# Kernel tuning notes

Hardware: AMD Instinct MI355X
Metric: run time of the kernel (lower is better)

## Reference

```python
import jax, jax.numpy as jnp
import numpy as np

B, N, M, K, C = 2, 4096, 4096, 32, 64
RADIUS = 0.08


def _ball_query(d2, radius, k):
    # d2: (B, N, M) squared distances. Returns (B, N, k) int32 indices of the
    # first k in-radius neighbors (in index order); empty slots are filled with
    # the first found neighbor (or 0 if none), matching standard ball_query.
    m = d2.shape[-1]
    mask = d2 < radius * radius
    ar = jnp.arange(m, dtype=jnp.int32)
    key = jnp.where(mask, ar, ar + m)          # in-radius indices sort first
    neg_vals, _ = jax.lax.top_k(-key, k)       # k smallest keys
    vals = -neg_vals
    valid = vals < m
    raw = vals % m
    fill = raw[..., :1]                        # first neighbor (0 if none)
    return jnp.where(valid, raw, fill)


def setup_inputs() -> dict:
    key = jax.random.key(0)
    ks = jax.random.split(key, 9)
    points = jax.random.uniform(ks[0], (B, 3, N), dtype=jnp.float32)
    knnpoints = jax.random.uniform(ks[1], (B, 3, M), dtype=jnp.float32)
    feat = jax.random.normal(ks[2], (B, C, M), dtype=jnp.float32)
    w1 = jax.random.normal(ks[3], (128, C + 4), dtype=jnp.float32) * 0.05
    b1 = jnp.zeros((128,), jnp.float32)
    w2 = jax.random.normal(ks[4], (64, 128), dtype=jnp.float32) * 0.05
    b2 = jnp.zeros((64,), jnp.float32)
    w3 = jax.random.normal(ks[5], (64, 64), dtype=jnp.float32) * 0.05
    b3 = jnp.zeros((64,), jnp.float32)
    return {"points": points, "knnpoints": knnpoints, "feat": feat,
            "w1": w1, "b1": b1, "w2": w2, "b2": b2, "w3": w3, "b3": b3}


def reference(points, knnpoints, feat, w1, b1, w2, b2, w3, b3):
    # pairwise squared distances (B, N, M), computed once and reused by
    # ball_query and ChamferLoss
    pe = jnp.sum(points ** 2, axis=1)                       # (B, N)
    ke = jnp.sum(knnpoints ** 2, axis=1)                    # (B, M)
    cross = jnp.einsum('bdn,bdm->bnm', points, knnpoints)
    d2 = jnp.maximum(pe[:, :, None] + ke[:, None, :] - 2.0 * cross, 0.0)

    idx = _ball_query(jax.lax.stop_gradient(d2), RADIUS, K)  # (B, N, K)

    # gather neighbor coords / features: knnpoints[j, :, idx[j]]
    nb = jax.vmap(lambda p, i: p[:, i])(knnpoints, idx)      # (B, 3, N, K)
    nf = jax.vmap(lambda f, i: f[:, i])(feat, idx)           # (B, C, N, K)

    # relation features (neighbor_feature): diff + squared distance
    diff = nb - points[:, :, :, None]                        # (B, 3, N, K)
    dist = jnp.sum(diff ** 2, axis=1, keepdims=True)         # (B, 1, N, K)
    x = jnp.concatenate([nf, diff, dist], axis=1)            # (B, C+4, N, K)

    # SharedMLP: 1x1 conv stacks + ReLU
    h = jax.nn.relu(jnp.einsum('oc,bcnk->bonk', w1, x) + b1[None, :, None, None])
    h = jax.nn.relu(jnp.einsum('oc,bcnk->bonk', w2, h) + b2[None, :, None, None])
    h = jax.nn.relu(jnp.einsum('oc,bcnk->bonk', w3, h) + b3[None, :, None, None])
    agg = jnp.sum(h, axis=3)                                 # (B, 64, N)

    # ChamferLoss between points and knnpoints
    cd = jnp.sqrt(1e-6 + d2)
    loss = jnp.min(cd, axis=1).mean() + jnp.min(cd, axis=2).mean()
    return agg, loss
```

## Files before the change

kernel.cpp:

```cpp
#include <hip/hip_runtime.h>
#include <cstdint>

#define BB 2
#define NN 4096
#define MM 4096
#define KK 32
#define CC 64
#define R2C 0.0064f

typedef _Float16 v8h __attribute__((ext_vector_type(8)));
typedef _Float16 v4h __attribute__((ext_vector_type(4)));
typedef float    v4f __attribute__((ext_vector_type(4)));

__launch_bounds__(256)
__global__ void setup_kernel(const float* __restrict__ points,
                             const float* __restrict__ knn,
                             const float* __restrict__ feat,
                             const float* __restrict__ w1,
                             const float* __restrict__ w2,
                             const float* __restrict__ w3,
                             float4* __restrict__ pointsT,
                             float4* __restrict__ knnT,
                             _Float16* __restrict__ featH,
                             _Float16* __restrict__ w1h,
                             _Float16* __restrict__ w2h,
                             _Float16* __restrict__ w3h,
                             float* __restrict__ lossbuf) {
    __shared__ float tile[64][65];
    int blk = blockIdx.x, t = threadIdx.x;
    if (blk < 64) {
        const float* src = (blk < 32) ? points : knn;
        float4* dst = (blk < 32) ? pointsT : knnT;
        int i = (blk & 31) * 256 + t;
        int b = i >> 12, p = i & 4095;
        const float* base = src + (size_t)b * 3 * 4096;
        float x = base[p], y = base[4096 + p], z = base[8192 + p];
        float e = __fadd_rn(__fadd_rn(__fmul_rn(x, x), __fmul_rn(y, y)),
                            __fmul_rn(z, z));
        dst[i] = make_float4(x, y, z, e);
    } else if (blk < 192) {
        int tb = blk - 64;
        int b = tb / (MM / 64);
        int m0 = (tb % (MM / 64)) * 64;
        int mi = t & 63, cq = t >> 6;
        const float* src = feat + (size_t)b * CC * MM;
#pragma unroll
        for (int r = 0; r < 16; ++r) {
            int c = cq * 16 + r;
            tile[mi][c] = src[(size_t)c * MM + m0 + mi];
        }
        __syncthreads();
        int ci = t & 63, mq = t >> 6;
        _Float16* dst = featH + ((size_t)b * MM + m0) * CC;
#pragma unroll
        for (int r = 0; r < 16; ++r) {
            int mm = mq * 16 + r;
            dst[(size_t)mm * CC + ci] = (_Float16)tile[mm][ci];
        }
    } else if (blk < 240) {
        int tt = (blk - 192) * 256 + t;
        if (tt < 128 * 96) {
            int r = tt / 96, k = tt - r * 96;
            w1h[tt] = (_Float16)((k < 68) ? w1[r * 68 + k] : 0.0f);
        }
        if (tt < 64 * 128) w2h[tt] = (_Float16)w2[tt];
        if (tt < 64 * 64)  w3h[tt] = (_Float16)w3[tt];
    } else {
        int i = ((blk - 240) * 256 + t) * 4;
        *(float4*)(lossbuf + i) = make_float4(0.f, 0.f, 0.f, 0.f);
    }
}

__launch_bounds__(256)
__global__ void scan_kernel(const float4* __restrict__ pointsT,
                            const float4* __restrict__ knnT,
                            int* __restrict__ idx_ws,
                            float* __restrict__ lossbuf) {
    __shared__ float4 tile[1024];
    __shared__ int sidx[16][KK];
    int t = threadIdx.x;
    int w = t >> 6, lane = t & 63;
    int blk = blockIdx.x;

    if (blk < 512) {
        int pt0 = blk * 16;
        int b = pt0 >> 12;
        float4 P[4];
#pragma unroll
        for (int p = 0; p < 4; ++p) P[p] = pointsT[pt0 + 4 * w + p];
        int cnt[4] = {0, 0, 0, 0};
        float mn[4] = {1e30f, 1e30f, 1e30f, 1e30f};
        const float4* kb = knnT + (size_t)b * MM;

        for (int ch = 0; ch < 4; ++ch) {
            const float4* src = kb + ch * 1024;
            tile[t] = src[t]; tile[t + 256] = src[t + 256];
            tile[t + 512] = src[t + 512]; tile[t + 768] = src[t + 768];
            __syncthreads();
#pragma unroll 2
            for (int i = 0; i < 16; ++i) {
                float4 k4 = tile[i * 64 + lane];
                int m = ch * 1024 + i * 64 + lane;
#pragma unroll
                for (int p = 0; p < 4; ++p) {
                    float cross = __builtin_fmaf(P[p].z, k4.z,
                                  __builtin_fmaf(P[p].y, k4.y,
                                                 __fmul_rn(P[p].x, k4.x)));
                    float d2 = __fsub_rn(__fadd_rn(P[p].w, k4.w),
                                         __fmul_rn(2.0f, cross));
                    mn[p] = fminf(mn[p], fmaxf(d2, 0.0f));
                    bool hit = d2 < R2C;
                    unsigned long long mask = __ballot(hit);
                    if (hit) {
                        int pos = cnt[p] + __builtin_amdgcn_mbcnt_hi(
                                     (unsigned)(mask >> 32),
                                     __builtin_amdgcn_mbcnt_lo((unsigned)mask, 0));
                        if (pos < KK) sidx[4 * w + p][pos] = m;
                    }
                    cnt[p] += __popcll(mask);
                }
            }
            __syncthreads();
        }

        float lsum = 0.0f;
#pragma unroll
        for (int p = 0; p < 4; ++p) {
            if (lane < KK) {
                int row = 4 * w + p;
                int fillv = (cnt[p] > 0) ? sidx[row][0] : 0;
                int v = (lane < cnt[p]) ? sidx[row][lane] : fillv;
                idx_ws[((size_t)(pt0 + row)) * KK + lane] = v;
            }
            float mv = mn[p];
            for (int off = 32; off > 0; off >>= 1)
                mv = fminf(mv, __shfl_xor(mv, off));
            lsum += sqrtf(1e-6f + mv);
        }
        if (lane == 0)
            atomicAdd(lossbuf + ((blk * 4 + w) & 1023) * 8,
                      lsum * (1.0f / (BB * NN)));
    } else {
        int blk2 = blk - 512;
        int m0 = blk2 * 16;
        int b = m0 >> 12;
        float4 Kp[4];
#pragma unroll
        for (int p = 0; p < 4; ++p) Kp[p] = knnT[m0 + 4 * w + p];
        float mn[4] = {1e30f, 1e30f, 1e30f, 1e30f};
        const float4* pb = pointsT + (size_t)b * NN;

        for (int ch = 0; ch < 4; ++ch) {
            const float4* src = pb + ch * 1024;
            tile[t] = src[t]; tile[t + 256] = src[t + 256];
            tile[t + 512] = src[t + 512]; tile[t + 768] = src[t + 768];
            __syncthreads();
#pragma unroll 2
            for (int i = 0; i < 16; ++i) {
                float4 p4 = tile[i * 64 + lane];
#pragma unroll
                for (int p = 0; p < 4; ++p) {
                    float cross = __builtin_fmaf(p4.z, Kp[p].z,
                                  __builtin_fmaf(p4.y, Kp[p].y,
                                                 __fmul_rn(p4.x, Kp[p].x)));
                    float d2 = __fsub_rn(__fadd_rn(p4.w, Kp[p].w),
                                         __fmul_rn(2.0f, cross));
                    mn[p] = fminf(mn[p], fmaxf(d2, 0.0f));
                }
            }
            __syncthreads();
        }

        float lsum = 0.0f;
#pragma unroll
        for (int p = 0; p < 4; ++p) {
            float mv = mn[p];
            for (int off = 32; off > 0; off >>= 1)
                mv = fminf(mv, __shfl_xor(mv, off));
            lsum += sqrtf(1e-6f + mv);
        }
        if (lane == 0)
            atomicAdd(lossbuf + ((blk2 * 4 + w) & 1023) * 8,
                      lsum * (1.0f / (BB * MM)));
    }
}

#define TC  64
#define XS  104
#define H1S 136
#define H2S 72

__launch_bounds__(256, 4)
__global__ void mlp_kernel(const float4* __restrict__ pointsT,
                           const float4* __restrict__ knnT,
                           const _Float16* __restrict__ featH,
                           const int* __restrict__ idx_ws,
                           const _Float16* __restrict__ w1h, const float* __restrict__ b1,
                           const _Float16* __restrict__ w2h, const float* __restrict__ b2,
                           const _Float16* __restrict__ w3h, const float* __restrict__ b3,
                           const float* __restrict__ lossbuf,
                           float* __restrict__ out) {
    __shared__ __align__(16) _Float16 SM[TC * XS + TC * H1S];
    _Float16* X  = SM;
    _Float16* H2 = SM;
    _Float16* H1 = SM + TC * XS;
    __shared__ float ws4[4];

    int t = threadIdx.x;

    if (blockIdx.x == 0) {
        float s = lossbuf[t * 8] + lossbuf[(t + 256) * 8] +
                  lossbuf[(t + 512) * 8] + lossbuf[(t + 768) * 8];
        for (int off = 32; off > 0; off >>= 1) s += __shfl_xor(s, off);
        if ((t & 63) == 0) ws4[t >> 6] = s;
        __syncthreads();
        if (t == 0)
            out[(size_t)BB * 64 * NN] = ws4[0] + ws4[1] + ws4[2] + ws4[3];
    }

    int point0 = blockIdx.x * 2;
    int b = point0 >> 12;
    int n0 = point0 & (NN - 1);

    {
        int col = t >> 2, h = t & 3;
        int pl = col >> 5, kk = col & 31;
        int n = n0 + pl;
        int id = idx_ws[(((size_t)b * NN + n) << 5) + kk];
        const v8h* src = (const v8h*)(featH + ((size_t)(b * MM + id)) * CC) + h * 2;
        v8h f0 = src[0], f1 = src[1];
        v8h* dst = (v8h*)(X + col * XS) + h * 2;
        dst[0] = f0; dst[1] = f1;
        v8h mv = {(_Float16)0.f, (_Float16)0.f, (_Float16)0.f, (_Float16)0.f,
                  (_Float16)0.f, (_Float16)0.f, (_Float16)0.f, (_Float16)0.f};
        if (h == 0) {
            float4 p4 = pointsT[b * NN + n];
            float4 nb = knnT[b * MM + id];
            float dx = nb.x - p4.x, dy = nb.y - p4.y, dz = nb.z - p4.z;
            float dd = __fadd_rn(__fadd_rn(__fmul_rn(dx, dx), __fmul_rn(dy, dy)),
                                 __fmul_rn(dz, dz));
            mv[0] = (_Float16)dx; mv[1] = (_Float16)dy;
            mv[2] = (_Float16)dz; mv[3] = (_Float16)dd;
        }
        *((v8h*)(X + col * XS + 64) + h) = mv;
    }

    int w = t >> 6, l = t & 63;
    int quad = l >> 4, lc = l & 15;

    v8h a1[2][3], a2[4], a3[2];
#pragma unroll
    for (int rt = 0; rt < 2; ++rt)
#pragma unroll
        for (int ks = 0; ks < 3; ++ks)
            a1[rt][ks] = *(const v8h*)(w1h + (32 * w + 16 * rt + lc) * 96 + 32 * ks + 8 * quad);
#pragma unroll
    for (int ks = 0; ks < 4; ++ks)
        a2[ks] = *(const v8h*)(w2h + (16 * w + lc) * 128 + 32 * ks + 8 * quad);
#pragma unroll
    for (int ks = 0; ks < 2; ++ks)
        a3[ks] = *(const v8h*)(w3h + (16 * w + lc) * 64 + 32 * ks + 8 * quad);

    v4f bias1a = *(const v4f*)(b1 + 32 * w + 4 * quad);
    v4f bias1b = *(const v4f*)(b1 + 32 * w + 16 + 4 * quad);
    v4f bias2  = *(const v4f*)(b2 + 16 * w + 4 * quad);
    v4f bias3  = *(const v4f*)(b3 + 16 * w + 4 * quad);

    __syncthreads();

#pragma unroll 1
    for (int ct = 0; ct < 4; ++ct) {
        int colb = 16 * ct + lc;
        v4f acc0 = bias1a, acc1 = bias1b;
#pragma unroll
        for (int ks = 0; ks < 3; ++ks) {
            v8h bx = *(const v8h*)(X + colb * XS + 32 * ks + 8 * quad);
            acc0 = __builtin_amdgcn_mfma_f32_16x16x32_f16(a1[0][ks], bx, acc0, 0, 0, 0);
            acc1 = __builtin_amdgcn_mfma_f32_16x16x32_f16(a1[1][ks], bx, acc1, 0, 0, 0);
        }
        v4h h0, h1v;
#pragma unroll
        for (int r = 0; r < 4; ++r) {
            h0[r]  = (_Float16)fmaxf(acc0[r], 0.0f);
            h1v[r] = (_Float16)fmaxf(acc1[r], 0.0f);
        }
        *(v4h*)(H1 + colb * H1S + 32 * w + 4 * quad)      = h0;
        *(v4h*)(H1 + colb * H1S + 32 * w + 16 + 4 * quad) = h1v;
    }
    __syncthreads();

#pragma unroll 1
    for (int ct = 0; ct < 4; ++ct) {
        int colb = 16 * ct + lc;
        v4f acc = bias2;
#pragma unroll
        for (int ks = 0; ks < 4; ++ks) {
            v8h bx = *(const v8h*)(H1 + colb * H1S + 32 * ks + 8 * quad);
            acc = __builtin_amdgcn_mfma_f32_16x16x32_f16(a2[ks], bx, acc, 0, 0, 0);
        }
        v4h h;
#pragma unroll
        for (int r = 0; r < 4; ++r) h[r] = (_Float16)fmaxf(acc[r], 0.0f);
        *(v4h*)(H2 + colb * H2S + 16 * w + 4 * quad) = h;
    }
    __syncthreads();

#pragma unroll 1
    for (int p = 0; p < 2; ++p) {
        int cA = (2 * p) * 16 + lc, cB = (2 * p + 1) * 16 + lc;
        v4f accA = bias3, accB = bias3;
#pragma unroll
        for (int ks = 0; ks < 2; ++ks) {
            v8h bA = *(const v8h*)(H2 + cA * H2S + 32 * ks + 8 * quad);
            v8h bB = *(const v8h*)(H2 + cB * H2S + 32 * ks + 8 * quad);
            accA = __builtin_amdgcn_mfma_f32_16x16x32_f16(a3[ks], bA, accA, 0, 0, 0);
            accB = __builtin_amdgcn_mfma_f32_16x16x32_f16(a3[ks], bB, accB, 0, 0, 0);
        }
        v4f s;
#pragma unroll
        for (int r = 0; r < 4; ++r)
            s[r] = fmaxf(accA[r], 0.0f) + fmaxf(accB[r], 0.0f);
#pragma unroll
        for (int off = 1; off < 16; off <<= 1) {
#pragma unroll
            for (int r = 0; r < 4; ++r) s[r] += __shfl_xor(s[r], off);
        }
        if (lc == 0) {
            int n = n0 + p;
            int rowb = 16 * w + 4 * quad;
#pragma unroll
            for (int r = 0; r < 4; ++r)
                out[((size_t)(b * 64 + rowb + r)) * NN + n] = s[r];
        }
    }
}

extern "C" void kernel_launch(void* const* d_in, const int* in_sizes, int n_in,
                              void* d_out, int out_size, void* d_ws, size_t ws_size,
                              hipStream_t stream) {
    const float* points = (const float*)d_in[0];
    const float* knn    = (const float*)d_in[1];
    const float* feat   = (const float*)d_in[2];
    const float* w1 = (const float*)d_in[3];
    const float* b1 = (const float*)d_in[4];
    const float* w2 = (const float*)d_in[5];
    const float* b2 = (const float*)d_in[6];
    const float* w3 = (const float*)d_in[7];
    const float* b3 = (const float*)d_in[8];
    float* out = (float*)d_out;

    char* ws = (char*)d_ws;
    float4*    pointsT = (float4*)ws;
    float4*    knnT    = (float4*)(ws + 131072);
    _Float16*  featH   = (_Float16*)(ws + 262144);
    int*       idx_ws  = (int*)(ws + 1310720);
    _Float16*  w1h     = (_Float16*)(ws + 2359296);
    _Float16*  w2h     = (_Float16*)(ws + 2383872);
    _Float16*  w3h     = (_Float16*)(ws + 2400256);
    float*     lossbuf = (float*)(ws + 2408448);

    setup_kernel<<<248, 256, 0, stream>>>(points, knn, feat, w1, w2, w3,
                                          pointsT, knnT, featH, w1h, w2h, w3h,
                                          lossbuf);
    scan_kernel<<<1024, 256, 0, stream>>>(pointsT, knnT, idx_ws, lossbuf);
    mlp_kernel<<<(BB * NN) / 2, 256, 0, stream>>>(pointsT, knnT, featH, idx_ws,
                                                  w1h, b1, w2h, b2, w3h, b3,
                                                  lossbuf, out);
}
```

Measured before the change: 121.4 us.

## Fuse ball-query scan and MLP into one kernel with last-block loss reduction

Merges the scan and MLP kernels so each ball-query block keeps its neighbor indices in shared memory and runs the three-layer MLP over its 16 points in 8 passes. This removes the idx_ws global round trip and one kernel launch. The final loss reduction moves to whichever block increments an atomic counter last. The trade-off is fewer, heavier blocks for the MLP phase (512 blocks doing 8 sequential passes instead of 4096 small blocks), which may hurt latency hiding. The fused kernel also has a larger shared-memory footprint and uses launch bounds of 4.

```diff
diff --git a/kernel.cpp b/kernel.cpp
--- a/kernel.cpp
+++ b/kernel.cpp
@@ -11,6 +11,11 @@
 typedef _Float16 v8h __attribute__((ext_vector_type(8)));
 typedef _Float16 v4h __attribute__((ext_vector_type(4)));
 typedef float    v4f __attribute__((ext_vector_type(4)));
+
+#define TC  64
+#define XS  104
+#define H1S 136
+#define H2S 72
 
 __launch_bounds__(256)
 __global__ void setup_kernel(const float* __restrict__ points,
@@ -25,7 +30,8 @@
                              _Float16* __restrict__ w1h,
                              _Float16* __restrict__ w2h,
                              _Float16* __restrict__ w3h,
-                             float* __restrict__ lossbuf) {
+                             float* __restrict__ lossbuf,
+                             int* __restrict__ counter) {
     __shared__ float tile[64][65];
     int blk = blockIdx.x, t = threadIdx.x;
     if (blk < 64) {
@@ -68,16 +74,29 @@
     } else {
         int i = ((blk - 240) * 256 + t) * 4;
         *(float4*)(lossbuf + i) = make_float4(0.f, 0.f, 0.f, 0.f);
+        if (blk == 240 && t == 0) counter[0] = 0;
     }
 }
 
-__launch_bounds__(256)
-__global__ void scan_kernel(const float4* __restrict__ pointsT,
-                            const float4* __restrict__ knnT,
-                            int* __restrict__ idx_ws,
-                            float* __restrict__ lossbuf) {
-    __shared__ float4 tile[1024];
+__launch_bounds__(256, 4)
+__global__ void fused_kernel(const float4* __restrict__ pointsT,
+                             const float4* __restrict__ knnT,
+                             const _Float16* __restrict__ featH,
+                             const _Float16* __restrict__ w1h, const float* __restrict__ b1,
+                             const _Float16* __restrict__ w2h, const float* __restrict__ b2,
+                             const _Float16* __restrict__ w3h, const float* __restrict__ b3,
+                             float* __restrict__ lossbuf,
+                             int* __restrict__ counter,
+                             float* __restrict__ out) {
+    __shared__ __align__(16) char SM[TC * XS * 2 + TC * H1S * 2];
     __shared__ int sidx[16][KK];
+    __shared__ float ws4v[4];
+    __shared__ int rflag;
+    float4*   tile = (float4*)SM;
+    _Float16* X    = (_Float16*)SM;
+    _Float16* H2   = (_Float16*)SM;
+    _Float16* H1   = (_Float16*)SM + TC * XS;
+
     int t = threadIdx.x;
     int w = t >> 6, lane = t & 63;
     int blk = blockIdx.x;
@@ -108,7 +127,7 @@
                                                  __fmul_rn(P[p].x, k4.x)));
                     float d2 = __fsub_rn(__fadd_rn(P[p].w, k4.w),
                                          __fmul_rn(2.0f, cross));
-                    mn[p] = fminf(mn[p], fmaxf(d2, 0.0f));
+                    mn[p] = fminf(mn[p], d2);
                     bool hit = d2 < R2C;
                     unsigned long long mask = __ballot(hit);
                     if (hit) {
@@ -126,20 +145,155 @@
         float lsum = 0.0f;
 #pragma unroll
         for (int p = 0; p < 4; ++p) {
+            int row = 4 * w + p;
             if (lane < KK) {
-                int row = 4 * w + p;
                 int fillv = (cnt[p] > 0) ? sidx[row][0] : 0;
-                int v = (lane < cnt[p]) ? sidx[row][lane] : fillv;
-                idx_ws[((size_t)(pt0 + row)) * KK + lane] = v;
+                if (lane >= cnt[p]) sidx[row][lane] = fillv;
             }
             float mv = mn[p];
             for (int off = 32; off > 0; off >>= 1)
                 mv = fminf(mv, __shfl_xor(mv, off));
-            lsum += sqrtf(1e-6f + mv);
+            lsum += sqrtf(1e-6f + fmaxf(mv, 0.0f));
         }
         if (lane == 0)
             atomicAdd(lossbuf + ((blk * 4 + w) & 1023) * 8,
                       lsum * (1.0f / (BB * NN)));
+        __syncthreads();
+        if (t == 0) {
+            __threadfence();
+            rflag = (atomicAdd(counter, 1) == 1023) ? 1 : 0;
+        }
+        __syncthreads();
+        if (rflag) {
+            float s = 0.0f;
+#pragma unroll
+            for (int q = 0; q < 4; ++q)
+                s += __hip_atomic_load(lossbuf + (t + 256 * q) * 8,
+                                       __ATOMIC_RELAXED, __HIP_MEMORY_SCOPE_AGENT);
+            for (int off = 32; off > 0; off >>= 1) s += __shfl_xor(s, off);
+            if ((t & 63) == 0) ws4v[t >> 6] = s;
+            __syncthreads();
+            if (t == 0)
+                out[(size_t)BB * 64 * NN] = ws4v[0] + ws4v[1] + ws4v[2] + ws4v[3];
+        }
+
+        int quad = lane >> 4, lc = lane & 15;
+        size_t bM = (size_t)b * MM;
+        int n0 = pt0;
+
+        v8h a1[2][3], a2[4], a3[2];
+#pragma unroll
+        for (int rt = 0; rt < 2; ++rt)
+#pragma unroll
+            for (int ks = 0; ks < 3; ++ks)
+                a1[rt][ks] = *(const v8h*)(w1h + (32 * w + 16 * rt + lc) * 96 + 32 * ks + 8 * quad);
+#pragma unroll
+        for (int ks = 0; ks < 4; ++ks)
+            a2[ks] = *(const v8h*)(w2h + (16 * w + lc) * 128 + 32 * ks + 8 * quad);
+#pragma unroll
+        for (int ks = 0; ks < 2; ++ks)
+            a3[ks] = *(const v8h*)(w3h + (16 * w + lc) * 64 + 32 * ks + 8 * quad);
+
+        v4f bias1a = *(const v4f*)(b1 + 32 * w + 4 * quad);
+        v4f bias1b = *(const v4f*)(b1 + 32 * w + 16 + 4 * quad);
+        v4f bias2  = *(const v4f*)(b2 + 16 * w + 4 * quad);
+        v4f bias3  = *(const v4f*)(b3 + 16 * w + 4 * quad);
+
+        __syncthreads();
+
+#pragma unroll 1
+        for (int ps = 0; ps < 8; ++ps) {
+            {
+                int col = t >> 2, h = t & 3;
+                int pl = col >> 5, kk = col & 31;
+                int lrow = 2 * ps + pl;
+                int id = sidx[lrow][kk];
+                const v8h* src = (const v8h*)(featH + (bM + id) * CC) + h * 2;
+                v8h f0 = src[0], f1 = src[1];
+                v8h* dst = (v8h*)(X + col * XS) + h * 2;
+                dst[0] = f0; dst[1] = f1;
+                v8h mv = {(_Float16)0.f, (_Float16)0.f, (_Float16)0.f, (_Float16)0.f,
+                          (_Float16)0.f, (_Float16)0.f, (_Float16)0.f, (_Float16)0.f};
+                if (h == 0) {
+                    float4 p4 = pointsT[n0 + lrow];
+                    float4 nb = knnT[bM + id];
+                    float dx = nb.x - p4.x, dy = nb.y - p4.y, dz = nb.z - p4.z;
+                    float dd = __fadd_rn(__fadd_rn(__fmul_rn(dx, dx), __fmul_rn(dy, dy)),
+                                         __fmul_rn(dz, dz));
+                    mv[0] = (_Float16)dx; mv[1] = (_Float16)dy;
+                    mv[2] = (_Float16)dz; mv[3] = (_Float16)dd;
+                }
+                *((v8h*)(X + col * XS + 64) + h) = mv;
+            }
+            __syncthreads();
+
+#pragma unroll 1
+            for (int ct = 0; ct < 4; ++ct) {
+                int colb = 16 * ct + lc;
+                v4f acc0 = bias1a, acc1 = bias1b;
+#pragma unroll
+                for (int ks = 0; ks < 3; ++ks) {
+                    v8h bx = *(const v8h*)(X + colb * XS + 32 * ks + 8 * quad);
+                    acc0 = __builtin_amdgcn_mfma_f32_16x16x32_f16(a1[0][ks], bx, acc0, 0, 0, 0);
+                    acc1 = __builtin_amdgcn_mfma_f32_16x16x32_f16(a1[1][ks], bx, acc1, 0, 0, 0);
+                }
+                v4h h0, h1v;
+#pragma unroll
+                for (int r = 0; r < 4; ++r) {
+                    h0[r]  = (_Float16)fmaxf(acc0[r], 0.0f);
+                    h1v[r] = (_Float16)fmaxf(acc1[r], 0.0f);
+                }
+                *(v4h*)(H1 + colb * H1S + 32 * w + 4 * quad)      = h0;
+                *(v4h*)(H1 + colb * H1S + 32 * w + 16 + 4 * quad) = h1v;
+            }
+            __syncthreads();
+
+#pragma unroll 1
+            for (int ct = 0; ct < 4; ++ct) {
+                int colb = 16 * ct + lc;
+                v4f acc = bias2;
+#pragma unroll
+                for (int ks = 0; ks < 4; ++ks) {
+                    v8h bx = *(const v8h*)(H1 + colb * H1S + 32 * ks + 8 * quad);
+                    acc = __builtin_amdgcn_mfma_f32_16x16x32_f16(a2[ks], bx, acc, 0, 0, 0);
+                }
+                v4h h;
+#pragma unroll
+                for (int r = 0; r < 4; ++r) h[r] = (_Float16)fmaxf(acc[r], 0.0f);
+                *(v4h*)(H2 + colb * H2S + 16 * w + 4 * quad) = h;
+            }
+            __syncthreads();
+
+#pragma unroll 1
+            for (int p = 0; p < 2; ++p) {
+                int cA = (2 * p) * 16 + lc, cB = (2 * p + 1) * 16 + lc;
+                v4f accA = bias3, accB = bias3;
+#pragma unroll
+                for (int ks = 0; ks < 2; ++ks) {
+                    v8h bA = *(const v8h*)(H2 + cA * H2S + 32 * ks + 8 * quad);
+                    v8h bB = *(const v8h*)(H2 + cB * H2S + 32 * ks + 8 * quad);
+                    accA = __builtin_amdgcn_mfma_f32_16x16x32_f16(a3[ks], bA, accA, 0, 0, 0);
+                    accB = __builtin_amdgcn_mfma_f32_16x16x32_f16(a3[ks], bB, accB, 0, 0, 0);
+                }
+                v4f s;
+#pragma unroll
+                for (int r = 0; r < 4; ++r)
+                    s[r] = fmaxf(accA[r], 0.0f) + fmaxf(accB[r], 0.0f);
+#pragma unroll
+                for (int off = 1; off < 16; off <<= 1) {
+#pragma unroll
+                    for (int r = 0; r < 4; ++r) s[r] += __shfl_xor(s[r], off);
+                }
+                if (lc == 0) {
+                    int nloc = (n0 & (NN - 1)) + 2 * ps + p;
+                    int rowb = 16 * w + 4 * quad;
+#pragma unroll
+                    for (int r = 0; r < 4; ++r)
+                        out[((size_t)(b * 64 + rowb + r)) * NN + nloc] = s[r];
+                }
+            }
+            __syncthreads();
+        }
     } else {
         int blk2 = blk - 512;
         int m0 = blk2 * 16;
@@ -165,7 +319,7 @@
                                                  __fmul_rn(p4.x, Kp[p].x)));
                     float d2 = __fsub_rn(__fadd_rn(p4.w, Kp[p].w),
                                          __fmul_rn(2.0f, cross));
-                    mn[p] = fminf(mn[p], fmaxf(d2, 0.0f));
+                    mn[p] = fminf(mn[p], d2);
                 }
             }
             __syncthreads();
@@ -177,160 +331,28 @@
             float mv = mn[p];
             for (int off = 32; off > 0; off >>= 1)
                 mv = fminf(mv, __shfl_xor(mv, off));
-            lsum += sqrtf(1e-6f + mv);
+            lsum += sqrtf(1e-6f + fmaxf(mv, 0.0f));
         }
         if (lane == 0)
             atomicAdd(lossbuf + ((blk2 * 4 + w) & 1023) * 8,
                       lsum * (1.0f / (BB * MM)));
-    }
-}
-
-#define TC  64
-#define XS  104
-#define H1S 136
-#define H2S 72
-
-__launch_bounds__(256, 4)
-__global__ void mlp_kernel(const float4* __restrict__ pointsT,
-                           const float4* __restrict__ knnT,
-                           const _Float16* __restrict__ featH,
-                           const int* __restrict__ idx_ws,
-                           const _Float16* __restrict__ w1h, const float* __restrict__ b1,
-                           const _Float16* __restrict__ w2h, const float* __restrict__ b2,
-                           const _Float16* __restrict__ w3h, const float* __restrict__ b3,
-                           const float* __restrict__ lossbuf,
-                           float* __restrict__ out) {
-    __shared__ __align__(16) _Float16 SM[TC * XS + TC * H1S];
-    _Float16* X  = SM;
-    _Float16* H2 = SM;
-    _Float16* H1 = SM + TC * XS;
-    __shared__ float ws4[4];
-
-    int t = threadIdx.x;
-
-    if (blockIdx.x == 0) {
-        float s = lossbuf[t * 8] + lossbuf[(t + 256) * 8] +
-                  lossbuf[(t + 512) * 8] + lossbuf[(t + 768) * 8];
-        for (int off = 32; off > 0; off >>= 1) s += __shfl_xor(s, off);
-        if ((t & 63) == 0) ws4[t >> 6] = s;
-        __syncthreads();
-        if (t == 0)
-            out[(size_t)BB * 64 * NN] = ws4[0] + ws4[1] + ws4[2] + ws4[3];
-    }
-
-    int point0 = blockIdx.x * 2;
-    int b = point0 >> 12;
-    int n0 = point0 & (NN - 1);
-
-    {
-        int col = t >> 2, h = t & 3;
-        int pl = col >> 5, kk = col & 31;
-        int n = n0 + pl;
-        int id = idx_ws[(((size_t)b * NN + n) << 5) + kk];
-        const v8h* src = (const v8h*)(featH + ((size_t)(b * MM + id)) * CC) + h * 2;
-        v8h f0 = src[0], f1 = src[1];
-        v8h* dst = (v8h*)(X + col * XS) + h * 2;
-        dst[0] = f0; dst[1] = f1;
-        v8h mv = {(_Float16)0.f, (_Float16)0.f, (_Float16)0.f, (_Float16)0.f,
-                  (_Float16)0.f, (_Float16)0.f, (_Float16)0.f, (_Float16)0.f};
-        if (h == 0) {
-            float4 p4 = pointsT[b * NN + n];
-            float4 nb = knnT[b * MM + id];
-            float dx = nb.x - p4.x, dy = nb.y - p4.y, dz = nb.z - p4.z;
-            float dd = __fadd_rn(__fadd_rn(__fmul_rn(dx, dx), __fmul_rn(dy, dy)),
-                                 __fmul_rn(dz, dz));
-            mv[0] = (_Float16)dx; mv[1] = (_Float16)dy;
-            mv[2] = (_Float16)dz; mv[3] = (_Float16)dd;
-        }
-        *((v8h*)(X + col * XS + 64) + h) = mv;
-    }
-
-    int w = t >> 6, l = t & 63;
-    int quad = l >> 4, lc = l & 15;
-
-    v8h a1[2][3], a2[4], a3[2];
-#pragma unroll
-    for (int rt = 0; rt < 2; ++rt)
-#pragma unroll
-        for (int ks = 0; ks < 3; ++ks)
-            a1[rt][ks] = *(const v8h*)(w1h + (32 * w + 16 * rt + lc) * 96 + 32 * ks + 8 * quad);
-#pragma unroll
-    for (int ks = 0; ks < 4; ++ks)
-        a2[ks] = *(const v8h*)(w2h + (16 * w + lc) * 128 + 32 * ks + 8 * quad);
-#pragma unroll
-    for (int ks = 0; ks < 2; ++ks)
-        a3[ks] = *(const v8h*)(w3h + (16 * w + lc) * 64 + 32 * ks + 8 * quad);
-
-    v4f bias1a = *(const v4f*)(b1 + 32 * w + 4 * quad);
-    v4f bias1b = *(const v4f*)(b1 + 32 * w + 16 + 4 * quad);
-    v4f bias2  = *(const v4f*)(b2 + 16 * w + 4 * quad);
-    v4f bias3  = *(const v4f*)(b3 + 16 * w + 4 * quad);
-
-    __syncthreads();
-
-#pragma unroll 1
-    for (int ct = 0; ct < 4; ++ct) {
-        int colb = 16 * ct + lc;
-        v4f acc0 = bias1a, acc1 = bias1b;
-#pragma unroll
-        for (int ks = 0; ks < 3; ++ks) {
-            v8h bx = *(const v8h*)(X + colb * XS + 32 * ks + 8 * quad);
-            acc0 = __builtin_amdgcn_mfma_f32_16x16x32_f16(a1[0][ks], bx, acc0, 0, 0, 0);
-            acc1 = __builtin_amdgcn_mfma_f32_16x16x32_f16(a1[1][ks], bx, acc1, 0, 0, 0);
-        }
-        v4h h0, h1v;
-#pragma unroll
-        for (int r = 0; r < 4; ++r) {
-            h0[r]  = (_Float16)fmaxf(acc0[r], 0.0f);
-            h1v[r] = (_Float16)fmaxf(acc1[r], 0.0f);
-        }
-        *(v4h*)(H1 + colb * H1S + 32 * w + 4 * quad)      = h0;
-        *(v4h*)(H1 + colb * H1S + 32 * w + 16 + 4 * quad) = h1v;
-    }
-    __syncthreads();
-
-#pragma unroll 1
-    for (int ct = 0; ct < 4; ++ct) {
-        int colb = 16 * ct + lc;
-        v4f acc = bias2;
-#pragma unroll
-        for (int ks = 0; ks < 4; ++ks) {
-            v8h bx = *(const v8h*)(H1 + colb * H1S + 32 * ks + 8 * quad);
-            acc = __builtin_amdgcn_mfma_f32_16x16x32_f16(a2[ks], bx, acc, 0, 0, 0);
-        }
-        v4h h;
-#pragma unroll
-        for (int r = 0; r < 4; ++r) h[r] = (_Float16)fmaxf(acc[r], 0.0f);
-        *(v4h*)(H2 + colb * H2S + 16 * w + 4 * quad) = h;
-    }
-    __syncthreads();
-
-#pragma unroll 1
-    for (int p = 0; p < 2; ++p) {
-        int cA = (2 * p) * 16 + lc, cB = (2 * p + 1) * 16 + lc;
-        v4f accA = bias3, accB = bias3;
-#pragma unroll
-        for (int ks = 0; ks < 2; ++ks) {
-            v8h bA = *(const v8h*)(H2 + cA * H2S + 32 * ks + 8 * quad);
-            v8h bB = *(const v8h*)(H2 + cB * H2S + 32 * ks + 8 * quad);
-            accA = __builtin_amdgcn_mfma_f32_16x16x32_f16(a3[ks], bA, accA, 0, 0, 0);
-            accB = __builtin_amdgcn_mfma_f32_16x16x32_f16(a3[ks], bB, accB, 0, 0, 0);
-        }
-        v4f s;
-#pragma unroll
-        for (int r = 0; r < 4; ++r)
-            s[r] = fmaxf(accA[r], 0.0f) + fmaxf(accB[r], 0.0f);
-#pragma unroll
-        for (int off = 1; off < 16; off <<= 1) {
-#pragma unroll
-            for (int r = 0; r < 4; ++r) s[r] += __shfl_xor(s[r], off);
-        }
-        if (lc == 0) {
-            int n = n0 + p;
-            int rowb = 16 * w + 4 * quad;
-#pragma unroll
-            for (int r = 0; r < 4; ++r)
-                out[((size_t)(b * 64 + rowb + r)) * NN + n] = s[r];
+        __syncthreads();
+        if (t == 0) {
+            __threadfence();
+            rflag = (atomicAdd(counter, 1) == 1023) ? 1 : 0;
+        }
+        __syncthreads();
+        if (rflag) {
+            float s = 0.0f;
+#pragma unroll
+            for (int q = 0; q < 4; ++q)
+                s += __hip_atomic_load(lossbuf + (t + 256 * q) * 8,
+                                       __ATOMIC_RELAXED, __HIP_MEMORY_SCOPE_AGENT);
+            for (int off = 32; off > 0; off >>= 1) s += __shfl_xor(s, off);
+            if ((t & 63) == 0) ws4v[t >> 6] = s;
+            __syncthreads();
+            if (t == 0)
+                out[(size_t)BB * 64 * NN] = ws4v[0] + ws4v[1] + ws4v[2] + ws4v[3];
         }
     }
 }
@@ -353,17 +375,16 @@
     float4*    pointsT = (float4*)ws;
     float4*    knnT    = (float4*)(ws + 131072);
     _Float16*  featH   = (_Float16*)(ws + 262144);
-    int*       idx_ws  = (int*)(ws + 1310720);
-    _Float16*  w1h     = (_Float16*)(ws + 2359296);
-    _Float16*  w2h     = (_Float16*)(ws + 2383872);
-    _Float16*  w3h     = (_Float16*)(ws + 2400256);
-    float*     lossbuf = (float*)(ws + 2408448);
+    _Float16*  w1h     = (_Float16*)(ws + 1310720);
+    _Float16*  w2h     = (_Float16*)(ws + 1335296);
+    _Float16*  w3h     = (_Float16*)(ws + 1351680);
+    float*     lossbuf = (float*)(ws + 1359872);
+    int*       counter = (int*)(ws + 1392640);
 
     setup_kernel<<<248, 256, 0, stream>>>(points, knn, feat, w1, w2, w3,
                                           pointsT, knnT, featH, w1h, w2h, w3h,
-                                          lossbuf);
-    scan_kernel<<<1024, 256, 0, stream>>>(pointsT, knnT, idx_ws, lossbuf);
-    mlp_kernel<<<(BB * NN) / 2, 256, 0, stream>>>(pointsT, knnT, featH, idx_ws,
-                                                  w1h, b1, w2h, b2, w3h, b3,
-                                                  lossbuf, out);
+                                          lossbuf, counter);
+    fused_kernel<<<1024, 256, 0, stream>>>(pointsT, knnT, featH,
+                                           w1h, b1, w2h, b2, w3h, b3,
+                                           lossbuf, counter, out);
 }
```

Measured after the change: 130.9 us. 7.8% more time.

## Fuse setup into scan kernel and compute point norms on the fly

Applied to the files above, without the earlier changes.

Merges the setup kernel into the scan kernel, so one launch and one inter-kernel dependency go away. The transposed float4 point copies are dropped: the scan and MLP kernels now read the SoA coordinates directly and recompute squared norms per tile. The loss partials are written to distinct slots instead of atomically added, which also removes the buffer zeroing, and the clamp to zero moves after the min reduction. In exchange each scan block does extra strided loads and norm arithmetic, and the feature and weight conversion blocks now run in the same grid as the scan blocks.

```diff
diff --git a/kernel.cpp b/kernel.cpp
--- a/kernel.cpp
+++ b/kernel.cpp
@@ -12,90 +12,58 @@
 typedef _Float16 v4h __attribute__((ext_vector_type(4)));
 typedef float    v4f __attribute__((ext_vector_type(4)));
 
+#define TC  64
+#define XS  104
+#define H1S 136
+#define H2S 72
+
 __launch_bounds__(256)
-__global__ void setup_kernel(const float* __restrict__ points,
-                             const float* __restrict__ knn,
-                             const float* __restrict__ feat,
-                             const float* __restrict__ w1,
-                             const float* __restrict__ w2,
-                             const float* __restrict__ w3,
-                             float4* __restrict__ pointsT,
-                             float4* __restrict__ knnT,
-                             _Float16* __restrict__ featH,
-                             _Float16* __restrict__ w1h,
-                             _Float16* __restrict__ w2h,
-                             _Float16* __restrict__ w3h,
-                             float* __restrict__ lossbuf) {
-    __shared__ float tile[64][65];
-    int blk = blockIdx.x, t = threadIdx.x;
-    if (blk < 64) {
-        const float* src = (blk < 32) ? points : knn;
-        float4* dst = (blk < 32) ? pointsT : knnT;
-        int i = (blk & 31) * 256 + t;
-        int b = i >> 12, p = i & 4095;
-        const float* base = src + (size_t)b * 3 * 4096;
-        float x = base[p], y = base[4096 + p], z = base[8192 + p];
-        float e = __fadd_rn(__fadd_rn(__fmul_rn(x, x), __fmul_rn(y, y)),
-                            __fmul_rn(z, z));
-        dst[i] = make_float4(x, y, z, e);
-    } else if (blk < 192) {
-        int tb = blk - 64;
-        int b = tb / (MM / 64);
-        int m0 = (tb % (MM / 64)) * 64;
-        int mi = t & 63, cq = t >> 6;
-        const float* src = feat + (size_t)b * CC * MM;
-#pragma unroll
-        for (int r = 0; r < 16; ++r) {
-            int c = cq * 16 + r;
-            tile[mi][c] = src[(size_t)c * MM + m0 + mi];
-        }
-        __syncthreads();
-        int ci = t & 63, mq = t >> 6;
-        _Float16* dst = featH + ((size_t)b * MM + m0) * CC;
-#pragma unroll
-        for (int r = 0; r < 16; ++r) {
-            int mm = mq * 16 + r;
-            dst[(size_t)mm * CC + ci] = (_Float16)tile[mm][ci];
-        }
-    } else if (blk < 240) {
-        int tt = (blk - 192) * 256 + t;
-        if (tt < 128 * 96) {
-            int r = tt / 96, k = tt - r * 96;
-            w1h[tt] = (_Float16)((k < 68) ? w1[r * 68 + k] : 0.0f);
-        }
-        if (tt < 64 * 128) w2h[tt] = (_Float16)w2[tt];
-        if (tt < 64 * 64)  w3h[tt] = (_Float16)w3[tt];
-    } else {
-        int i = ((blk - 240) * 256 + t) * 4;
-        *(float4*)(lossbuf + i) = make_float4(0.f, 0.f, 0.f, 0.f);
-    }
-}
-
-__launch_bounds__(256)
-__global__ void scan_kernel(const float4* __restrict__ pointsT,
-                            const float4* __restrict__ knnT,
-                            int* __restrict__ idx_ws,
-                            float* __restrict__ lossbuf) {
-    __shared__ float4 tile[1024];
+__global__ void scan_setup_kernel(const float* __restrict__ points,
+                                  const float* __restrict__ knn,
+                                  const float* __restrict__ feat,
+                                  const float* __restrict__ w1,
+                                  const float* __restrict__ w2,
+                                  const float* __restrict__ w3,
+                                  _Float16* __restrict__ featH,
+                                  _Float16* __restrict__ w1h,
+                                  _Float16* __restrict__ w2h,
+                                  _Float16* __restrict__ w3h,
+                                  int* __restrict__ idx_ws,
+                                  float* __restrict__ lossbuf) {
+    __shared__ __align__(16) char SM[16640];
     __shared__ int sidx[16][KK];
+    float4* tile = (float4*)SM;
     int t = threadIdx.x;
     int w = t >> 6, lane = t & 63;
     int blk = blockIdx.x;
 
     if (blk < 512) {
         int pt0 = blk * 16;
-        int b = pt0 >> 12;
+        int b = blk >> 8;
+        const float* pp = points + (size_t)b * 3 * NN;
+        const float* kp = knn + (size_t)b * 3 * MM;
         float4 P[4];
 #pragma unroll
-        for (int p = 0; p < 4; ++p) P[p] = pointsT[pt0 + 4 * w + p];
+        for (int p = 0; p < 4; ++p) {
+            int nl = (pt0 & (NN - 1)) + 4 * w + p;
+            float x = pp[nl], y = pp[NN + nl], z = pp[2 * NN + nl];
+            float e = __fadd_rn(__fadd_rn(__fmul_rn(x, x), __fmul_rn(y, y)),
+                                __fmul_rn(z, z));
+            P[p] = make_float4(x, y, z, e);
+        }
         int cnt[4] = {0, 0, 0, 0};
         float mn[4] = {1e30f, 1e30f, 1e30f, 1e30f};
-        const float4* kb = knnT + (size_t)b * MM;
 
         for (int ch = 0; ch < 4; ++ch) {
-            const float4* src = kb + ch * 1024;
-            tile[t] = src[t]; tile[t + 256] = src[t + 256];
-            tile[t + 512] = src[t + 512]; tile[t + 768] = src[t + 768];
+            const float* kx = kp + ch * 1024;
+#pragma unroll
+            for (int j = 0; j < 4; ++j) {
+                int i = t + 256 * j;
+                float x = kx[i], y = kx[MM + i], z = kx[2 * MM + i];
+                float e = __fadd_rn(__fadd_rn(__fmul_rn(x, x), __fmul_rn(y, y)),
+                                    __fmul_rn(z, z));
+                tile[i] = make_float4(x, y, z, e);
+            }
             __syncthreads();
 #pragma unroll 2
             for (int i = 0; i < 16; ++i) {
@@ -108,7 +76,7 @@
                                                  __fmul_rn(P[p].x, k4.x)));
                     float d2 = __fsub_rn(__fadd_rn(P[p].w, k4.w),
                                          __fmul_rn(2.0f, cross));
-                    mn[p] = fminf(mn[p], fmaxf(d2, 0.0f));
+                    mn[p] = fminf(mn[p], d2);
                     bool hit = d2 < R2C;
                     unsigned long long mask = __ballot(hit);
                     if (hit) {
@@ -126,8 +94,8 @@
         float lsum = 0.0f;
 #pragma unroll
         for (int p = 0; p < 4; ++p) {
+            int row = 4 * w + p;
             if (lane < KK) {
-                int row = 4 * w + p;
                 int fillv = (cnt[p] > 0) ? sidx[row][0] : 0;
                 int v = (lane < cnt[p]) ? sidx[row][lane] : fillv;
                 idx_ws[((size_t)(pt0 + row)) * KK + lane] = v;
@@ -135,25 +103,37 @@
             float mv = mn[p];
             for (int off = 32; off > 0; off >>= 1)
                 mv = fminf(mv, __shfl_xor(mv, off));
-            lsum += sqrtf(1e-6f + mv);
+            lsum += sqrtf(1e-6f + fmaxf(mv, 0.0f));
         }
         if (lane == 0)
-            atomicAdd(lossbuf + ((blk * 4 + w) & 1023) * 8,
-                      lsum * (1.0f / (BB * NN)));
-    } else {
+            lossbuf[blk * 4 + w] = lsum * (1.0f / (BB * NN));
+    } else if (blk < 1024) {
         int blk2 = blk - 512;
         int m0 = blk2 * 16;
-        int b = m0 >> 12;
+        int b = blk2 >> 8;
+        const float* pp = points + (size_t)b * 3 * NN;
+        const float* kp = knn + (size_t)b * 3 * MM;
         float4 Kp[4];
 #pragma unroll
-        for (int p = 0; p < 4; ++p) Kp[p] = knnT[m0 + 4 * w + p];
+        for (int p = 0; p < 4; ++p) {
+            int ml = (m0 & (MM - 1)) + 4 * w + p;
+            float x = kp[ml], y = kp[MM + ml], z = kp[2 * MM + ml];
+            float e = __fadd_rn(__fadd_rn(__fmul_rn(x, x), __fmul_rn(y, y)),
+                                __fmul_rn(z, z));
+            Kp[p] = make_float4(x, y, z, e);
+        }
         float mn[4] = {1e30f, 1e30f, 1e30f, 1e30f};
-        const float4* pb = pointsT + (size_t)b * NN;
 
         for (int ch = 0; ch < 4; ++ch) {
-            const float4* src = pb + ch * 1024;
-            tile[t] = src[t]; tile[t + 256] = src[t + 256];
-            tile[t + 512] = src[t + 512]; tile[t + 768] = src[t + 768];
+            const float* px = pp + ch * 1024;
+#pragma unroll
+            for (int j = 0; j < 4; ++j) {
+                int i = t + 256 * j;
+                float x = px[i], y = px[NN + i], z = px[2 * NN + i];
+                float e = __fadd_rn(__fadd_rn(__fmul_rn(x, x), __fmul_rn(y, y)),
+                                    __fmul_rn(z, z));
+                tile[i] = make_float4(x, y, z, e);
+            }
             __syncthreads();
 #pragma unroll 2
             for (int i = 0; i < 16; ++i) {
@@ -165,7 +145,7 @@
                                                  __fmul_rn(p4.x, Kp[p].x)));
                     float d2 = __fsub_rn(__fadd_rn(p4.w, Kp[p].w),
                                          __fmul_rn(2.0f, cross));
-                    mn[p] = fminf(mn[p], fmaxf(d2, 0.0f));
+                    mn[p] = fminf(mn[p], d2);
                 }
             }
             __syncthreads();
@@ -177,22 +157,44 @@
             float mv = mn[p];
             for (int off = 32; off > 0; off >>= 1)
                 mv = fminf(mv, __shfl_xor(mv, off));
-            lsum += sqrtf(1e-6f + mv);
+            lsum += sqrtf(1e-6f + fmaxf(mv, 0.0f));
         }
         if (lane == 0)
-            atomicAdd(lossbuf + ((blk2 * 4 + w) & 1023) * 8,
-                      lsum * (1.0f / (BB * MM)));
+            lossbuf[2048 + blk2 * 4 + w] = lsum * (1.0f / (BB * MM));
+    } else if (blk < 1152) {
+        float (*tl)[65] = (float (*)[65])SM;
+        int tb = blk - 1024;
+        int b = tb / (MM / 64);
+        int m0 = (tb % (MM / 64)) * 64;
+        int mi = t & 63, cq = t >> 6;
+        const float* src = feat + (size_t)b * CC * MM;
+#pragma unroll
+        for (int r = 0; r < 16; ++r) {
+            int c = cq * 16 + r;
+            tl[mi][c] = src[(size_t)c * MM + m0 + mi];
+        }
+        __syncthreads();
+        int ci = t & 63, mq = t >> 6;
+        _Float16* dst = featH + ((size_t)b * MM + m0) * CC;
+#pragma unroll
+        for (int r = 0; r < 16; ++r) {
+            int mm = mq * 16 + r;
+            dst[(size_t)mm * CC + ci] = (_Float16)tl[mm][ci];
+        }
+    } else {
+        int tt = (blk - 1152) * 256 + t;
+        if (tt < 128 * 96) {
+            int r = tt / 96, k = tt - r * 96;
+            w1h[tt] = (_Float16)((k < 68) ? w1[r * 68 + k] : 0.0f);
+        }
+        if (tt < 64 * 128) w2h[tt] = (_Float16)w2[tt];
+        if (tt < 64 * 64)  w3h[tt] = (_Float16)w3[tt];
     }
 }
 
-#define TC  64
-#define XS  104
-#define H1S 136
-#define H2S 72
-
 __launch_bounds__(256, 4)
-__global__ void mlp_kernel(const float4* __restrict__ pointsT,
-                           const float4* __restrict__ knnT,
+__global__ void mlp_kernel(const float* __restrict__ points,
+                           const float* __restrict__ knn,
                            const _Float16* __restrict__ featH,
                            const int* __restrict__ idx_ws,
                            const _Float16* __restrict__ w1h, const float* __restrict__ b1,
@@ -209,8 +211,9 @@
     int t = threadIdx.x;
 
     if (blockIdx.x == 0) {
-        float s = lossbuf[t * 8] + lossbuf[(t + 256) * 8] +
-                  lossbuf[(t + 512) * 8] + lossbuf[(t + 768) * 8];
+        float s = 0.0f;
+#pragma unroll
+        for (int q = 0; q < 16; ++q) s += lossbuf[t + 256 * q];
         for (int off = 32; off > 0; off >>= 1) s += __shfl_xor(s, off);
         if ((t & 63) == 0) ws4[t >> 6] = s;
         __syncthreads();
@@ -221,6 +224,8 @@
     int point0 = blockIdx.x * 2;
     int b = point0 >> 12;
     int n0 = point0 & (NN - 1);
+    const float* pp = points + (size_t)b * 3 * NN;
+    const float* kp = knn + (size_t)b * 3 * MM;
 
     {
         int col = t >> 2, h = t & 3;
@@ -234,9 +239,9 @@
         v8h mv = {(_Float16)0.f, (_Float16)0.f, (_Float16)0.f, (_Float16)0.f,
                   (_Float16)0.f, (_Float16)0.f, (_Float16)0.f, (_Float16)0.f};
         if (h == 0) {
-            float4 p4 = pointsT[b * NN + n];
-            float4 nb = knnT[b * MM + id];
-            float dx = nb.x - p4.x, dy = nb.y - p4.y, dz = nb.z - p4.z;
+            float px = pp[n], py = pp[NN + n], pz = pp[2 * NN + n];
+            float kx = kp[id], ky = kp[MM + id], kz = kp[2 * MM + id];
+            float dx = kx - px, dy = ky - py, dz = kz - pz;
             float dd = __fadd_rn(__fadd_rn(__fmul_rn(dx, dx), __fmul_rn(dy, dy)),
                                  __fmul_rn(dz, dz));
             mv[0] = (_Float16)dx; mv[1] = (_Float16)dy;
@@ -350,20 +355,17 @@
     float* out = (float*)d_out;
 
     char* ws = (char*)d_ws;
-    float4*    pointsT = (float4*)ws;
-    float4*    knnT    = (float4*)(ws + 131072);
-    _Float16*  featH   = (_Float16*)(ws + 262144);
-    int*       idx_ws  = (int*)(ws + 1310720);
-    _Float16*  w1h     = (_Float16*)(ws + 2359296);
-    _Float16*  w2h     = (_Float16*)(ws + 2383872);
-    _Float16*  w3h     = (_Float16*)(ws + 2400256);
-    float*     lossbuf = (float*)(ws + 2408448);
-
-    setup_kernel<<<248, 256, 0, stream>>>(points, knn, feat, w1, w2, w3,
-                                          pointsT, knnT, featH, w1h, w2h, w3h,
-                                          lossbuf);
-    scan_kernel<<<1024, 256, 0, stream>>>(pointsT, knnT, idx_ws, lossbuf);
-    mlp_kernel<<<(BB * NN) / 2, 256, 0, stream>>>(pointsT, knnT, featH, idx_ws,
+    _Float16*  featH   = (_Float16*)ws;
+    int*       idx_ws  = (int*)(ws + 1048576);
+    _Float16*  w1h     = (_Float16*)(ws + 2097152);
+    _Float16*  w2h     = (_Float16*)(ws + 2121728);
+    _Float16*  w3h     = (_Float16*)(ws + 2138112);
+    float*     lossbuf = (float*)(ws + 2146304);
+
+    scan_setup_kernel<<<1200, 256, 0, stream>>>(points, knn, feat, w1, w2, w3,
+                                                featH, w1h, w2h, w3h,
+                                                idx_ws, lossbuf);
+    mlp_kernel<<<(BB * NN) / 2, 256, 0, stream>>>(points, knn, featH, idx_ws,
                                                   w1h, b1, w2h, b2, w3h, b3,
                                                   lossbuf, out);
 }
```

Result: no change. 119.4 us, median of 2 (-1.7%).
